# Optimization experiments

Measured on AMD Instinct MI355X. Metric: run time of the kernel, lower is better.

Reference implementation:

```python
import jax, jax.numpy as jnp
import numpy as np

EMB_SZ, NHID, NLAYERS, NTOK = 400, 1150, 3, 32000


def _lstm_layer(x, w_ih, w_hh, b_ih, b_hh):
    # x: [S, B, in]; w_ih: [4H, in]; w_hh: [4H, H]; gate order i, f, g, o (PyTorch)
    S, B, _ = x.shape
    H = w_hh.shape[1]
    # precompute input contributions for all timesteps (one big GEMM)
    xg = jnp.einsum('sbi,gi->sbg', x, w_ih) + b_ih + b_hh  # [S, B, 4H]

    def step(carry, xt):
        h, c = carry
        g = xt + h @ w_hh.T  # [B, 4H]
        i, f, gg, o = jnp.split(g, 4, axis=-1)
        i = jax.nn.sigmoid(i)
        f = jax.nn.sigmoid(f)
        gg = jnp.tanh(gg)
        o = jax.nn.sigmoid(o)
        c = f * c + i * gg
        h = o * jnp.tanh(c)
        return (h, c), h

    init = (jnp.zeros((B, H), x.dtype), jnp.zeros((B, H), x.dtype))
    _, ys = jax.lax.scan(step, init, xg)
    return ys  # [S, B, H]


def setup_inputs() -> dict:
    key = jax.random.key(0)
    ks = jax.random.split(key, 16)
    S, B = 512, 64
    x = jax.random.randint(ks[0], (S, B), 0, NTOK, dtype=jnp.int64) if jax.config.jax_enable_x64 else jax.random.randint(ks[0], (S, B), 0, NTOK, dtype=jnp.int32)
    initrange = 0.1
    emb = jax.random.uniform(ks[1], (NTOK, EMB_SZ), jnp.float32, -initrange, initrange)
    emb = emb.at[1].set(0.0)  # padding_idx = 1
    dims = [(EMB_SZ, NHID), (NHID, NHID), (NHID, EMB_SZ)]  # (input, hidden) per layer
    d = {"x": x, "emb": emb}
    for l, (din, h) in enumerate(dims):
        s = 1.0 / np.sqrt(h)
        d[f"w_ih{l}"] = jax.random.uniform(ks[2 + 4 * l], (4 * h, din), jnp.float32, -s, s)
        d[f"w_hh{l}"] = jax.random.uniform(ks[3 + 4 * l], (4 * h, h), jnp.float32, -s, s)
        d[f"b_ih{l}"] = jax.random.uniform(ks[4 + 4 * l], (4 * h,), jnp.float32, -s, s)
        d[f"b_hh{l}"] = jax.random.uniform(ks[5 + 4 * l], (4 * h,), jnp.float32, -s, s)
    return d


def reference(x, emb, w_ih0, w_hh0, b_ih0, b_hh0, w_ih1, w_hh1, b_ih1, b_hh1, w_ih2, w_hh2, b_ih2, b_hh2):
    # eval mode: embedding dropout / locked dropout / weight-drop are all identity
    h = emb[x]  # [S, B, emb_sz]
    h = _lstm_layer(h, w_ih0, w_hh0, b_ih0, b_hh0)  # [S, B, nhid]
    h = _lstm_layer(h, w_ih1, w_hh1, b_ih1, b_hh1)  # [S, B, nhid]
    h = _lstm_layer(h, w_ih2, w_hh2, b_ih2, b_hh2)  # [S, B, emb_sz]
    return h
```

## Files before the change

### kernel.cpp

```cpp
#include <hip/hip_runtime.h>
#include <stdint.h>

typedef _Float16 f16x8 __attribute__((ext_vector_type(8)));
typedef _Float16 f16x4 __attribute__((ext_vector_type(4)));
typedef float f32x4 __attribute__((ext_vector_type(4)));

static __device__ __forceinline__ float bf2f(unsigned short u) {
  return __uint_as_float(((unsigned int)u) << 16);
}
static __device__ __forceinline__ unsigned short f2bf(float f) {
  unsigned int u = __float_as_uint(f);
  u = (u + 0x7FFFu + ((u >> 16) & 1u)) >> 16;
  return (unsigned short)u;
}
static __device__ __forceinline__ unsigned short f2h(float f) {
  _Float16 h = (_Float16)f;
  return __builtin_bit_cast(unsigned short, h);
}
static __device__ __forceinline__ float h2f(unsigned short b) {
  _Float16 h = __builtin_bit_cast(_Float16, b);
  return (float)h;
}
static __device__ __forceinline__ float sigm(float x) { return 1.0f / (1.0f + __expf(-x)); }
static __device__ __forceinline__ float tanh_fast(float x) {
  float ax = fabsf(x);
  float e = __expf(-2.0f * ax);
  float r = (1.0f - e) / (1.0f + e);
  return copysignf(r, x);
}

__global__ void probe_kernel(const unsigned int* __restrict__ raw, unsigned int* __restrict__ dflag) {
  __shared__ int s;
  int tid = threadIdx.x;
  if (tid == 0) s = 0;
  __syncthreads();
  int v = 0;
  for (int k = 0; k < 4; ++k) {
    unsigned int d = raw[2048 + tid * 4 + k];
    unsigned int lo = d & 0xFFFFu, ex = (lo >> 7) & 0xFFu;
    if (lo == 0u || (ex >= 0x40u && ex <= 0x7Cu)) v++;
  }
  atomicAdd(&s, v);
  __syncthreads();
  if (tid == 0) dflag[0] = (s >= 614) ? 1u : 0u;
}

__global__ void embed_kernel(const int* __restrict__ x, const void* __restrict__ emb,
                             unsigned short* __restrict__ act, const unsigned int* __restrict__ dflag) {
  int idx = blockIdx.x * 256 + threadIdx.x;
  int row = idx / 56, c = idx % 56;
  unsigned short* dst = act + (size_t)row * 448 + c * 8;
  union { uint4 v; unsigned short s[8]; } o;
  if (c < 50) {
    int tok = x[row];
    if (dflag[0]) {
      const unsigned short* e = (const unsigned short*)emb + (size_t)tok * 400 + c * 8;
      union { uint4 v; unsigned short s[8]; } r; r.v = *(const uint4*)e;
#pragma unroll
      for (int k = 0; k < 8; ++k) o.s[k] = f2h(bf2f(r.s[k]));
    } else {
      const float* e = (const float*)emb + (size_t)tok * 400 + c * 8;
      float4 r0 = *(const float4*)e, r1 = *(const float4*)(e + 4);
      const float* p0 = (const float*)&r0; const float* p1 = (const float*)&r1;
#pragma unroll
      for (int k = 0; k < 4; ++k) { o.s[k] = f2h(p0[k]); o.s[4 + k] = f2h(p1[k]); }
    }
  } else {
    o.v.x = o.v.y = o.v.z = o.v.w = 0u;
  }
  *(uint4*)dst = o.v;
}

__global__ void prep_kernel(const void* __restrict__ wih, const void* __restrict__ whh,
                            const void* __restrict__ bih, const void* __restrict__ bhh,
                            unsigned short* __restrict__ WihG, unsigned short* __restrict__ WhhG,
                            float* __restrict__ biasG, int H, int HPo, int din, int dpIn,
                            const unsigned int* __restrict__ dflag) {
  int nb = 4 * HPo, bid = blockIdx.x, tid = threadIdx.x;
  bool isf32 = (dflag[0] == 0u);
  if (bid < 2 * nb) {
    bool ih = bid < nb;
    int j = ih ? bid : bid - nb;
    int i = (j >> 6) * 16 + (j & 15), q = (j >> 4) & 3;
    int cdst = ih ? dpIn : HPo, csrc = ih ? din : H;
    unsigned short* dst = (ih ? WihG : WhhG) + (size_t)j * cdst;
    bool valid = i < H;
    const void* w = ih ? wih : whh;
    for (int m = tid; m < cdst; m += 256) {
      unsigned short v = 0;
      if (valid && m < csrc) {
        if (isf32) v = f2h(((const float*)w)[(size_t)(q * H + i) * csrc + m]);
        else       v = f2h(bf2f(((const unsigned short*)w)[(size_t)(q * H + i) * csrc + m]));
      }
      dst[m] = v;
    }
  } else {
    for (int m = tid; m < nb; m += 256) {
      int i = (m >> 6) * 16 + (m & 15), q = (m >> 4) & 3;
      float v = 0.0f;
      if (i < H) {
        if (isf32) v = ((const float*)bih)[q * H + i] + ((const float*)bhh)[q * H + i];
        else       v = bf2f(((const unsigned short*)bih)[q * H + i]) + bf2f(((const unsigned short*)bhh)[q * H + i]);
      }
      biasG[m] = v;
    }
  }
}

__global__ void unpad_kernel(const unsigned short* __restrict__ act, void* __restrict__ out,
                             const unsigned int* __restrict__ dflag) {
  int idx = blockIdx.x * 256 + threadIdx.x;
  int row = idx / 50, c = idx % 50;
  const unsigned short* src = act + (size_t)row * 448 + c * 8;
  union { uint4 v; unsigned short s[8]; } u; u.v = *(const uint4*)src;
  if (dflag[0]) {
    union { uint4 v; unsigned short s[8]; } o;
#pragma unroll
    for (int k = 0; k < 8; ++k) o.s[k] = f2bf(h2f(u.s[k]));
    *(uint4*)((unsigned short*)out + (size_t)row * 400 + c * 8) = o.v;
  } else {
    float4 o0, o1;
    float* p0 = (float*)&o0; float* p1 = (float*)&o1;
#pragma unroll
    for (int k = 0; k < 4; ++k) { p0[k] = h2f(u.s[k]); p1[k] = h2f(u.s[4 + k]); }
    float* dst = (float*)out + (size_t)row * 400 + c * 8;
    *(float4*)dst = o0; *(float4*)(dst + 4) = o1;
  }
}

__global__ __launch_bounds__(256, 1) void gemm_xw_kernel(
    const unsigned short* __restrict__ A, const unsigned short* __restrict__ B,
    unsigned short* __restrict__ gx, int K, int chrows) {
  __shared__ unsigned short Asm[128 * 32], Bsm[128 * 32];
  const int tid = threadIdx.x, lane = tid & 63, wv = tid >> 6;
  const int bm0 = blockIdx.x * 128, bn0 = blockIdx.y * 128;
  f32x4 acc[2][8] = {};
  const int nkt = K >> 5;
  for (int kt = 0; kt < nkt; ++kt) {
    __syncthreads();
#pragma unroll
    for (int j = 0; j < 2; ++j) {
      int idx = tid * 2 + j, r = idx >> 2, c4 = idx & 3;
      uint4 va = *(const uint4*)(A + (size_t)(bm0 + r) * K + kt * 32 + c4 * 8);
      uint4 vb = *(const uint4*)(B + (size_t)(bn0 + r) * K + kt * 32 + c4 * 8);
      int off = (r * 64 + c4 * 16) ^ ((r & 7) << 4);
      *(uint4*)((char*)Asm + off) = va;
      *(uint4*)((char*)Bsm + off) = vb;
    }
    __syncthreads();
    f16x8 af[2], bf[8];
#pragma unroll
    for (int rt = 0; rt < 2; ++rt) {
      int arow = wv * 32 + rt * 16 + (lane & 15);
      int off = (arow * 64 + ((lane >> 4) << 4)) ^ ((arow & 7) << 4);
      af[rt] = *(const f16x8*)((char*)Asm + off);
    }
#pragma unroll
    for (int ct = 0; ct < 8; ++ct) {
      int brow = ct * 16 + (lane & 15);
      int off = (brow * 64 + ((lane >> 4) << 4)) ^ ((brow & 7) << 4);
      bf[ct] = *(const f16x8*)((char*)Bsm + off);
    }
#pragma unroll
    for (int rt = 0; rt < 2; ++rt)
#pragma unroll
      for (int ct = 0; ct < 8; ++ct)
        acc[rt][ct] = __builtin_amdgcn_mfma_f32_16x16x32_f16(af[rt], bf[ct], acc[rt][ct], 0, 0, 0);
  }
#pragma unroll
  for (int ct = 0; ct < 8; ++ct) {
    int n = bn0 + ct * 16 + (lane & 15);
    int G = n >> 6, c = n & 63;
    int cellcol = (c & 15) * 4 + (c >> 4);
#pragma unroll
    for (int rt = 0; rt < 2; ++rt) {
#pragma unroll
      for (int reg = 0; reg < 4; ++reg) {
        int m = bm0 + wv * 32 + rt * 16 + ((lane >> 4) << 2) + reg;
        gx[((size_t)G * chrows + m) * 64 + cellcol] = f2h(acc[rt][ct][reg]);
      }
    }
  }
}

template <int HP, int KQW, int NQ, int NCNT>
static __device__ __forceinline__ void rec_body(
    const unsigned short* __restrict__ gxAll, unsigned short* __restrict__ actOut,
    const unsigned short* __restrict__ WhhG, const float* __restrict__ biasG,
    unsigned int* __restrict__ cnt, float* __restrict__ cstate,
    int t0, int TS, int chrows) {
  constexpr int NB = HP / 16;
  constexpr unsigned PERQ = (unsigned)(NB / NCNT);
  constexpr int KS = HP / KQW;
  constexpr int KT = KS / 32;
  constexpr int CF = 4 / NQ;
  constexpr int GSTR = 68;
  extern __shared__ char smem[];
  float* Gp = (float*)smem;
  const int tid = threadIdx.x, lane = tid & 63, wv = tid >> 6;
  const int kq = wv % KQW, t2 = wv / KQW;
  const int nq = t2 % NQ, mh = t2 / NQ;
  const int lrow = lane & 15, kc8 = (lane >> 4) << 3;
  const int G = blockIdx.x >> 1, bh = blockIdx.x & 1;
  const int urow = tid >> 4, ui = tid & 15;
  unsigned int* mycnt = cnt + (size_t)bh * 8 * 32;

  float bs[4];
  float creg = 0.0f;
  f16x8 wreg[CF][KT];
  {
    const unsigned short* wbase = WhhG + (size_t)G * 64 * HP + kq * KS + kc8;
#pragma unroll
    for (int cf = 0; cf < CF; ++cf) {
      const unsigned short* wp = wbase + (size_t)((nq * CF + cf) * 16 + lrow) * HP;
#pragma unroll
      for (int kt = 0; kt < KT; ++kt) wreg[cf][kt] = *(const f16x8*)(wp + kt * 32);
    }
#pragma unroll
    for (int q = 0; q < 4; ++q) bs[q] = biasG[G * 64 + q * 16 + ui];
    if (t0 > 0) creg = cstate[(bh * 32 + urow) * HP + G * 16 + ui];
  }
  __syncthreads();

  const int tend = t0 + TS;
  for (int t = t0; t < tend; ++t) {
    if (t > 0) {
      while (true) {
        int ok = 1;
        if (tid < NCNT)
          ok = (__hip_atomic_load(mycnt + tid * 32, __ATOMIC_RELAXED, __HIP_MEMORY_SCOPE_AGENT) >= PERQ * (unsigned)t);
        if (__syncthreads_and(ok)) break;
        __builtin_amdgcn_s_sleep(1);
      }
      asm volatile("" ::: "memory");
    }
    f16x4 gxv = *(const f16x4*)(gxAll + ((size_t)G * chrows + (t - t0) * 64 + bh * 32 + urow) * 64 + ui * 4);
    if (t > 0) {
      f16x8 hv[KT];
      const unsigned short* hp =
          actOut + ((size_t)(t - 1) * 64 + bh * 32 + mh * 16 + lrow) * HP + kq * KS + kc8;
#pragma unroll
      for (int kt = 0; kt < KT; ++kt) hv[kt] = *(const f16x8*)(hp + kt * 32);
      f32x4 a[CF];
#pragma unroll
      for (int cf = 0; cf < CF; ++cf) a[cf] = f32x4{0.f, 0.f, 0.f, 0.f};
#pragma unroll
      for (int kt = 0; kt < KT; ++kt)
#pragma unroll
        for (int cf = 0; cf < CF; ++cf)
          a[cf] = __builtin_amdgcn_mfma_f32_16x16x32_f16(hv[kt], wreg[cf][kt], a[cf], 0, 0, 0);
      const int br = kq * 32 + mh * 16 + (lane >> 4) * 4;
#pragma unroll
      for (int cf = 0; cf < CF; ++cf)
#pragma unroll
        for (int r = 0; r < 4; ++r)
          Gp[(br + r) * GSTR + (nq * CF + cf) * 16 + (lane & 15)] = a[cf][r];
    }
    asm volatile("s_waitcnt lgkmcnt(0)" ::: "memory");
    __builtin_amdgcn_s_barrier();
    __builtin_amdgcn_sched_barrier(0);
    float gi = (float)gxv[0] + bs[0], gf = (float)gxv[1] + bs[1];
    float gg = (float)gxv[2] + bs[2], go = (float)gxv[3] + bs[3];
    if (t > 0) {
#pragma unroll
      for (int k = 0; k < KQW; ++k) {
        const int base = (k * 32 + urow) * GSTR + ui;
        gi += Gp[base];
        gf += Gp[base + 16];
        gg += Gp[base + 32];
        go += Gp[base + 48];
      }
    }
    float ig = sigm(gi), fg = sigm(gf), gt = tanh_fast(gg), og = sigm(go);
    creg = fg * creg + ig * gt;
    unsigned short hb = f2h(og * tanh_fast(creg));
    int other = __shfl_xor((int)hb, 1);
    if ((ui & 1) == 0) {
      unsigned int pk = ((unsigned)hb & 0xFFFFu) | ((unsigned)other << 16);
      __hip_atomic_store((unsigned int*)(actOut + ((size_t)t * 64 + bh * 32 + urow) * HP + G * 16 + ui),
                         pk, __ATOMIC_RELAXED, __HIP_MEMORY_SCOPE_AGENT);
    }
    asm volatile("s_waitcnt vmcnt(0)" ::: "memory");
    __syncthreads();
    if (tid == 0)
      __hip_atomic_fetch_add(mycnt + (G % NCNT) * 32, 1u, __ATOMIC_RELEASE, __HIP_MEMORY_SCOPE_AGENT);
  }
  cstate[(bh * 32 + urow) * HP + G * 16 + ui] = creg;
}

__global__ __launch_bounds__(512, 1) void lstm_rec1152(
    const unsigned short* __restrict__ gxAll, unsigned short* __restrict__ actOut,
    const unsigned short* __restrict__ WhhG, const float* __restrict__ biasG,
    unsigned int* __restrict__ cnt, float* __restrict__ cstate, int t0, int TS, int chrows) {
  rec_body<1152, 4, 1, 8>(gxAll, actOut, WhhG, biasG, cnt, cstate, t0, TS, chrows);
}
__global__ __launch_bounds__(512, 1) void lstm_rec448(
    const unsigned short* __restrict__ gxAll, unsigned short* __restrict__ actOut,
    const unsigned short* __restrict__ WhhG, const float* __restrict__ biasG,
    unsigned int* __restrict__ cnt, float* __restrict__ cstate, int t0, int TS, int chrows) {
  rec_body<448, 2, 2, 4>(gxAll, actOut, WhhG, biasG, cnt, cstate, t0, TS, chrows);
}

extern "C" void kernel_launch(void* const* d_in, const int* in_sizes, int n_in,
                              void* d_out, int out_size, void* d_ws, size_t ws_size,
                              hipStream_t stream) {
  (void)in_sizes; (void)n_in; (void)out_size;
  const int* x = (const int*)d_in[0];
  const void* emb = d_in[1];
  const void* wih[3] = {d_in[2], d_in[6], d_in[10]};
  const void* whh[3] = {d_in[3], d_in[7], d_in[11]};
  const void* bih[3] = {d_in[4], d_in[8], d_in[12]};
  const void* bhh[3] = {d_in[5], d_in[9], d_in[13]};

  char* ws = (char*)d_ws;
  size_t off = 0;
  unsigned short* act0 = (unsigned short*)(ws + off); off += (size_t)32768 * 448 * 2;
  unsigned short* act1 = (unsigned short*)(ws + off); off += (size_t)32768 * 1152 * 2;
  unsigned short* act2 = (unsigned short*)(ws + off); off += (size_t)32768 * 1152 * 2;
  unsigned short* act3 = act0;
  unsigned short* WihG = (unsigned short*)(ws + off); off += (size_t)4608 * 1152 * 2;
  unsigned short* WhhG = (unsigned short*)(ws + off); off += (size_t)4608 * 1152 * 2;
  float* biasG = (float*)(ws + off); off += (size_t)4608 * 4;
  float* cstate = (float*)(ws + off); off += (size_t)64 * 1152 * 4;
  unsigned int* cnt = (unsigned int*)(ws + off); off += 4096;
  unsigned int* dflag = (unsigned int*)(ws + off); off += 256;
  unsigned short* gx = (unsigned short*)(ws + off);

  size_t avail = (ws_size > off) ? (ws_size - off) : 0;
  int CH = 512;
  while (CH > 32 && (size_t)CH * 589824 > avail) CH >>= 1;
  const int chrows = CH * 64, nch = 512 / CH;

  const size_t lds1152 = 128 * 68 * 4;
  const size_t lds448 = 64 * 68 * 4;

  probe_kernel<<<1, 256, 0, stream>>>((const unsigned int*)emb, dflag);
  embed_kernel<<<7168, 256, 0, stream>>>(x, emb, act0, dflag);

  prep_kernel<<<2 * 4608 + 1, 256, 0, stream>>>(wih[0], whh[0], bih[0], bhh[0],
                                                WihG, WhhG, biasG, 1150, 1152, 400, 448, dflag);
  hipMemsetAsync(cnt, 0, 4096, stream);
  for (int c = 0; c < nch; ++c) {
    gemm_xw_kernel<<<dim3(CH / 2, 36), 256, 0, stream>>>(act0 + (size_t)c * chrows * 448, WihG, gx, 448, chrows);
    lstm_rec1152<<<144, 512, lds1152, stream>>>(gx, act1, WhhG, biasG, cnt, cstate, c * CH, CH, chrows);
  }

  prep_kernel<<<2 * 4608 + 1, 256, 0, stream>>>(wih[1], whh[1], bih[1], bhh[1],
                                                WihG, WhhG, biasG, 1150, 1152, 1150, 1152, dflag);
  hipMemsetAsync(cnt, 0, 4096, stream);
  for (int c = 0; c < nch; ++c) {
    gemm_xw_kernel<<<dim3(CH / 2, 36), 256, 0, stream>>>(act1 + (size_t)c * chrows * 1152, WihG, gx, 1152, chrows);
    lstm_rec1152<<<144, 512, lds1152, stream>>>(gx, act2, WhhG, biasG, cnt, cstate, c * CH, CH, chrows);
  }

  prep_kernel<<<2 * 1792 + 1, 256, 0, stream>>>(wih[2], whh[2], bih[2], bhh[2],
                                                WihG, WhhG, biasG, 400, 448, 1150, 1152, dflag);
  hipMemsetAsync(cnt, 0, 4096, stream);
  for (int c = 0; c < nch; ++c) {
    gemm_xw_kernel<<<dim3(CH / 2, 14), 256, 0, stream>>>(act2 + (size_t)c * chrows * 1152, WihG, gx, 1152, chrows);
    lstm_rec448<<<56, 512, lds448, stream>>>(gx, act3, WhhG, biasG, cnt, cstate, c * CH, CH, chrows);
  }

  unpad_kernel<<<6400, 256, 0, stream>>>(act3, d_out, dflag);
}
```

Measured before the change: 10.04 ms.

## Split batch into four 16-row quarters and pipeline recurrent LSTM halves per block

Each recurrent block now handles two 16-row batch quarters instead of one 32-row half. All 8 waves split K across all 4 gates, and quarters A and B are processed in a staggered way. Quarter B's hidden-state loads and MFMA overlap with quarter A's gate reduction and counter signaling, so dependent blocks can start sooner. This adds extra barriers, counter polls and LDS traffic per timestep, and uses an uneven K split (4/5 or 2/1 k-tiles per wave) that can leave waves imbalanced.

New measurement: 11.34 ms. 1.13x slower.

```diff
diff --git a/kernel.cpp b/kernel.cpp
--- a/kernel.cpp
+++ b/kernel.cpp
@@ -183,88 +183,94 @@
   }
 }
 
-template <int HP, int KQW, int NQ, int NCNT>
+template <int KT>
+static __device__ __forceinline__ void loadh(f16x8* hv, const unsigned short* hp) {
+#pragma unroll
+  for (int kt = 0; kt < KT; ++kt) hv[kt] = *(const f16x8*)(hp + kt * 32);
+}
+template <int KT, int KTM>
+static __device__ __forceinline__ void loadw(f16x8 wreg[4][KTM], const unsigned short* wp, int HP) {
+#pragma unroll
+  for (int cf = 0; cf < 4; ++cf)
+#pragma unroll
+    for (int kt = 0; kt < KT; ++kt)
+      wreg[cf][kt] = *(const f16x8*)(wp + (size_t)cf * 16 * HP + kt * 32);
+}
+template <int KT, int KTM>
+static __device__ __forceinline__ void mmaq(const f16x8* hv, const f16x8 wreg[4][KTM], f32x4 acc[4]) {
+#pragma unroll
+  for (int kt = 0; kt < KT; ++kt)
+#pragma unroll
+    for (int cf = 0; cf < 4; ++cf)
+      acc[cf] = __builtin_amdgcn_mfma_f32_16x16x32_f16(hv[kt], wreg[cf][kt], acc[cf], 0, 0, 0);
+}
+
+template <int HP, int NA, int KTa, int KTb, int NCNT>
 static __device__ __forceinline__ void rec_body(
     const unsigned short* __restrict__ gxAll, unsigned short* __restrict__ actOut,
     const unsigned short* __restrict__ WhhG, const float* __restrict__ biasG,
     unsigned int* __restrict__ cnt, float* __restrict__ cstate,
-    int t0, int TS, int chrows) {
-  constexpr int NB = HP / 16;
-  constexpr unsigned PERQ = (unsigned)(NB / NCNT);
-  constexpr int KS = HP / KQW;
-  constexpr int KT = KS / 32;
-  constexpr int CF = 4 / NQ;
-  constexpr int GSTR = 68;
+    int t0, int TS, int chrows, int bid) {
+  constexpr int NGRP = HP / 16;
+  constexpr unsigned PERQ = (unsigned)(NGRP / NCNT);
+  constexpr int KTM = (KTa > KTb) ? KTa : KTb;
+  constexpr int GSTR = 72;
   extern __shared__ char smem[];
   float* Gp = (float*)smem;
   const int tid = threadIdx.x, lane = tid & 63, wv = tid >> 6;
-  const int kq = wv % KQW, t2 = wv / KQW;
-  const int nq = t2 % NQ, mh = t2 / NQ;
   const int lrow = lane & 15, kc8 = (lane >> 4) << 3;
-  const int G = blockIdx.x >> 1, bh = blockIdx.x & 1;
-  const int urow = tid >> 4, ui = tid & 15;
-  unsigned int* mycnt = cnt + (size_t)bh * 8 * 32;
-
-  float bs[4];
-  float creg = 0.0f;
-  f16x8 wreg[CF][KT];
+  const int G = bid >> 1, pr = bid & 1;
+  const int qa = pr * 2, qb = pr * 2 + 1;
+  const int kq = wv;
+  const int k0 = (kq < NA) ? kq * KTa * 32 : NA * KTa * 32 + (kq - NA) * KTb * 32;
+  const bool red = tid < 256;
+  const int urow = (tid >> 4) & 15, ui = tid & 15;
+  unsigned int* cntA = cnt + qa * 256;
+  unsigned int* cntB = cnt + qb * 256;
+
+  f16x8 wreg[4][KTM];
   {
-    const unsigned short* wbase = WhhG + (size_t)G * 64 * HP + kq * KS + kc8;
-#pragma unroll
-    for (int cf = 0; cf < CF; ++cf) {
-      const unsigned short* wp = wbase + (size_t)((nq * CF + cf) * 16 + lrow) * HP;
-#pragma unroll
-      for (int kt = 0; kt < KT; ++kt) wreg[cf][kt] = *(const f16x8*)(wp + kt * 32);
-    }
+    const unsigned short* wp = WhhG + ((size_t)(G * 64 + lrow)) * HP + k0 + kc8;
+    if (kq < NA) loadw<KTa, KTM>(wreg, wp, HP);
+    else         loadw<KTb, KTM>(wreg, wp, HP);
+  }
+  float bs[4] = {0.f, 0.f, 0.f, 0.f};
+  float cA = 0.f, cB = 0.f;
+  if (red) {
 #pragma unroll
     for (int q = 0; q < 4; ++q) bs[q] = biasG[G * 64 + q * 16 + ui];
-    if (t0 > 0) creg = cstate[(bh * 32 + urow) * HP + G * 16 + ui];
+    if (t0 > 0) {
+      cA = cstate[(qa * 16 + urow) * HP + G * 16 + ui];
+      cB = cstate[(qb * 16 + urow) * HP + G * 16 + ui];
+    }
   }
   __syncthreads();
 
-  const int tend = t0 + TS;
-  for (int t = t0; t < tend; ++t) {
-    if (t > 0) {
-      while (true) {
-        int ok = 1;
-        if (tid < NCNT)
-          ok = (__hip_atomic_load(mycnt + tid * 32, __ATOMIC_RELAXED, __HIP_MEMORY_SCOPE_AGENT) >= PERQ * (unsigned)t);
-        if (__syncthreads_and(ok)) break;
-        __builtin_amdgcn_s_sleep(1);
-      }
-      asm volatile("" ::: "memory");
-    }
-    f16x4 gxv = *(const f16x4*)(gxAll + ((size_t)G * chrows + (t - t0) * 64 + bh * 32 + urow) * 64 + ui * 4);
-    if (t > 0) {
-      f16x8 hv[KT];
-      const unsigned short* hp =
-          actOut + ((size_t)(t - 1) * 64 + bh * 32 + mh * 16 + lrow) * HP + kq * KS + kc8;
-#pragma unroll
-      for (int kt = 0; kt < KT; ++kt) hv[kt] = *(const f16x8*)(hp + kt * 32);
-      f32x4 a[CF];
-#pragma unroll
-      for (int cf = 0; cf < CF; ++cf) a[cf] = f32x4{0.f, 0.f, 0.f, 0.f};
-#pragma unroll
-      for (int kt = 0; kt < KT; ++kt)
-#pragma unroll
-        for (int cf = 0; cf < CF; ++cf)
-          a[cf] = __builtin_amdgcn_mfma_f32_16x16x32_f16(hv[kt], wreg[cf][kt], a[cf], 0, 0, 0);
-      const int br = kq * 32 + mh * 16 + (lane >> 4) * 4;
-#pragma unroll
-      for (int cf = 0; cf < CF; ++cf)
-#pragma unroll
-        for (int r = 0; r < 4; ++r)
-          Gp[(br + r) * GSTR + (nq * CF + cf) * 16 + (lane & 15)] = a[cf][r];
-    }
-    asm volatile("s_waitcnt lgkmcnt(0)" ::: "memory");
-    __builtin_amdgcn_s_barrier();
-    __builtin_amdgcn_sched_barrier(0);
+  auto pollq = [&](unsigned int* cq, unsigned need) {
+    while (true) {
+      int ok = 1;
+      if (tid < NCNT)
+        ok = (__hip_atomic_load(cq + tid * 32, __ATOMIC_RELAXED, __HIP_MEMORY_SCOPE_AGENT) >= need);
+      if (__syncthreads_and(ok)) break;
+      __builtin_amdgcn_s_sleep(1);
+    }
+    asm volatile("" ::: "memory");
+  };
+  auto stGp = [&](f32x4 acc[4]) {
+    const int br = kq * 16 + (lane >> 4) * 4;
+#pragma unroll
+    for (int cf = 0; cf < 4; ++cf)
+#pragma unroll
+      for (int r = 0; r < 4; ++r)
+        Gp[(br + r) * GSTR + cf * 16 + lrow] = acc[cf][r];
+  };
+  auto reduceq = [&](int q, int t, float& cc, f16x4 gxv, bool useGp) {
     float gi = (float)gxv[0] + bs[0], gf = (float)gxv[1] + bs[1];
     float gg = (float)gxv[2] + bs[2], go = (float)gxv[3] + bs[3];
-    if (t > 0) {
-#pragma unroll
-      for (int k = 0; k < KQW; ++k) {
-        const int base = (k * 32 + urow) * GSTR + ui;
+    if (useGp) {
+#pragma unroll
+      for (int k = 0; k < 8; ++k) {
+        const int base = (k * 16 + urow) * GSTR + ui;
         gi += Gp[base];
         gf += Gp[base + 16];
         gg += Gp[base + 32];
@@ -272,33 +278,78 @@
       }
     }
     float ig = sigm(gi), fg = sigm(gf), gt = tanh_fast(gg), og = sigm(go);
-    creg = fg * creg + ig * gt;
-    unsigned short hb = f2h(og * tanh_fast(creg));
+    cc = fg * cc + ig * gt;
+    unsigned short hb = f2h(og * tanh_fast(cc));
     int other = __shfl_xor((int)hb, 1);
     if ((ui & 1) == 0) {
       unsigned int pk = ((unsigned)hb & 0xFFFFu) | ((unsigned)other << 16);
-      __hip_atomic_store((unsigned int*)(actOut + ((size_t)t * 64 + bh * 32 + urow) * HP + G * 16 + ui),
+      __hip_atomic_store((unsigned int*)(actOut + ((size_t)t * 64 + q * 16 + urow) * HP + G * 16 + ui),
                          pk, __ATOMIC_RELAXED, __HIP_MEMORY_SCOPE_AGENT);
     }
+  };
+
+  const int tend = t0 + TS;
+  for (int t = t0; t < tend; ++t) {
+    const int tr = t - t0;
+    if (t > 0) pollq(cntA, PERQ * (unsigned)t);
+    f16x4 gxa = {}, gxb = {};
+    if (red) {
+      gxa = *(const f16x4*)(gxAll + ((size_t)G * chrows + tr * 64 + qa * 16 + urow) * 64 + ui * 4);
+      gxb = *(const f16x4*)(gxAll + ((size_t)G * chrows + tr * 64 + qb * 16 + urow) * 64 + ui * 4);
+    }
+    if (t > 0) {
+      f16x8 hv[KTM];
+      const unsigned short* hpA = actOut + ((size_t)(t - 1) * 64 + qa * 16 + lrow) * HP + k0 + kc8;
+      f32x4 acc[4] = {};
+      if (kq < NA) { loadh<KTa>(hv, hpA); mmaq<KTa, KTM>(hv, wreg, acc); }
+      else         { loadh<KTb>(hv, hpA); mmaq<KTb, KTM>(hv, wreg, acc); }
+      stGp(acc);
+    }
+    if (t > 0) pollq(cntB, PERQ * (unsigned)t);
+    else __syncthreads();
+    f16x8 hvB[KTM];
+    if (t > 0) {
+      const unsigned short* hpB = actOut + ((size_t)(t - 1) * 64 + qb * 16 + lrow) * HP + k0 + kc8;
+      if (kq < NA) loadh<KTa>(hvB, hpB);
+      else         loadh<KTb>(hvB, hpB);
+    }
+    if (red) reduceq(qa, t, cA, gxa, t > 0);
     asm volatile("s_waitcnt vmcnt(0)" ::: "memory");
     __syncthreads();
     if (tid == 0)
-      __hip_atomic_fetch_add(mycnt + (G % NCNT) * 32, 1u, __ATOMIC_RELEASE, __HIP_MEMORY_SCOPE_AGENT);
-  }
-  cstate[(bh * 32 + urow) * HP + G * 16 + ui] = creg;
+      __hip_atomic_fetch_add(cntA + (G & (NCNT - 1)) * 32, 1u, __ATOMIC_RELEASE, __HIP_MEMORY_SCOPE_AGENT);
+    if (t > 0) {
+      f32x4 acc[4] = {};
+      if (kq < NA) mmaq<KTa, KTM>(hvB, wreg, acc);
+      else         mmaq<KTb, KTM>(hvB, wreg, acc);
+      stGp(acc);
+    }
+    asm volatile("s_waitcnt lgkmcnt(0)" ::: "memory");
+    __builtin_amdgcn_s_barrier();
+    __builtin_amdgcn_sched_barrier(0);
+    if (red) reduceq(qb, t, cB, gxb, t > 0);
+    asm volatile("s_waitcnt vmcnt(0)" ::: "memory");
+    __syncthreads();
+    if (tid == 0)
+      __hip_atomic_fetch_add(cntB + (G & (NCNT - 1)) * 32, 1u, __ATOMIC_RELEASE, __HIP_MEMORY_SCOPE_AGENT);
+  }
+  if (red) {
+    cstate[(qa * 16 + urow) * HP + G * 16 + ui] = cA;
+    cstate[(qb * 16 + urow) * HP + G * 16 + ui] = cB;
+  }
 }
 
 __global__ __launch_bounds__(512, 1) void lstm_rec1152(
     const unsigned short* __restrict__ gxAll, unsigned short* __restrict__ actOut,
     const unsigned short* __restrict__ WhhG, const float* __restrict__ biasG,
     unsigned int* __restrict__ cnt, float* __restrict__ cstate, int t0, int TS, int chrows) {
-  rec_body<1152, 4, 1, 8>(gxAll, actOut, WhhG, biasG, cnt, cstate, t0, TS, chrows);
+  rec_body<1152, 4, 4, 5, 8>(gxAll, actOut, WhhG, biasG, cnt, cstate, t0, TS, chrows, blockIdx.x);
 }
 __global__ __launch_bounds__(512, 1) void lstm_rec448(
     const unsigned short* __restrict__ gxAll, unsigned short* __restrict__ actOut,
     const unsigned short* __restrict__ WhhG, const float* __restrict__ biasG,
     unsigned int* __restrict__ cnt, float* __restrict__ cstate, int t0, int TS, int chrows) {
-  rec_body<448, 2, 2, 4>(gxAll, actOut, WhhG, biasG, cnt, cstate, t0, TS, chrows);
+  rec_body<448, 6, 2, 1, 4>(gxAll, actOut, WhhG, biasG, cnt, cstate, t0, TS, chrows, blockIdx.x);
 }
 
 extern "C" void kernel_launch(void* const* d_in, const int* in_sizes, int n_in,
@@ -331,8 +382,7 @@
   while (CH > 32 && (size_t)CH * 589824 > avail) CH >>= 1;
   const int chrows = CH * 64, nch = 512 / CH;
 
-  const size_t lds1152 = 128 * 68 * 4;
-  const size_t lds448 = 64 * 68 * 4;
+  const size_t ldsrec = 128 * 72 * 4;
 
   probe_kernel<<<1, 256, 0, stream>>>((const unsigned int*)emb, dflag);
   embed_kernel<<<7168, 256, 0, stream>>>(x, emb, act0, dflag);
@@ -342,7 +392,7 @@
   hipMemsetAsync(cnt, 0, 4096, stream);
   for (int c = 0; c < nch; ++c) {
     gemm_xw_kernel<<<dim3(CH / 2, 36), 256, 0, stream>>>(act0 + (size_t)c * chrows * 448, WihG, gx, 448, chrows);
-    lstm_rec1152<<<144, 512, lds1152, stream>>>(gx, act1, WhhG, biasG, cnt, cstate, c * CH, CH, chrows);
+    lstm_rec1152<<<144, 512, ldsrec, stream>>>(gx, act1, WhhG, biasG, cnt, cstate, c * CH, CH, chrows);
   }
 
   prep_kernel<<<2 * 4608 + 1, 256, 0, stream>>>(wih[1], whh[1], bih[1], bhh[1],
@@ -350,7 +400,7 @@
   hipMemsetAsync(cnt, 0, 4096, stream);
   for (int c = 0; c < nch; ++c) {
     gemm_xw_kernel<<<dim3(CH / 2, 36), 256, 0, stream>>>(act1 + (size_t)c * chrows * 1152, WihG, gx, 1152, chrows);
-    lstm_rec1152<<<144, 512, lds1152, stream>>>(gx, act2, WhhG, biasG, cnt, cstate, c * CH, CH, chrows);
+    lstm_rec1152<<<144, 512, ldsrec, stream>>>(gx, act2, WhhG, biasG, cnt, cstate, c * CH, CH, chrows);
   }
 
   prep_kernel<<<2 * 1792 + 1, 256, 0, stream>>>(wih[2], whh[2], bih[2], bhh[2],
@@ -358,7 +408,7 @@
   hipMemsetAsync(cnt, 0, 4096, stream);
   for (int c = 0; c < nch; ++c) {
     gemm_xw_kernel<<<dim3(CH / 2, 14), 256, 0, stream>>>(act2 + (size_t)c * chrows * 1152, WihG, gx, 1152, chrows);
-    lstm_rec448<<<56, 512, lds448, stream>>>(gx, act3, WhhG, biasG, cnt, cstate, c * CH, CH, chrows);
+    lstm_rec448<<<56, 512, ldsrec, stream>>>(gx, act3, WhhG, biasG, cnt, cstate, c * CH, CH, chrows);
   }
 
   unpad_kernel<<<6400, 256, 0, stream>>>(act3, d_out, dflag);
```

## Repartition 1152-wide LSTM recurrence into 24-unit groups across 192 blocks

Applied to the files above, without the earlier changes.

The 1152-hidden recurrent kernel is rewritten so each block owns 24 hidden units (96 gate rows) for a 16-row batch quarter, giving 192 blocks instead of 144. All 8 waves split the K dimension unevenly (160/128) and hold the weights in registers, and the partial sums are reduced through a larger static LDS tile. The weight, bias and gx layouts are generalized to a configurable group width, so prep and the input GEMM emit a 96-wide gate interleave for layers 0 and 1. The aim is more CUs working on each sequential timestep and more work per wave. In exchange it uses more register pressure and more sync counters per step, and the batch quarters now each need their own barrier.

Result: no change. 9.896 ms (-1.4%).

```diff
diff --git a/kernel.cpp b/kernel.cpp
--- a/kernel.cpp
+++ b/kernel.cpp
@@ -74,14 +74,16 @@
 __global__ void prep_kernel(const void* __restrict__ wih, const void* __restrict__ whh,
                             const void* __restrict__ bih, const void* __restrict__ bhh,
                             unsigned short* __restrict__ WihG, unsigned short* __restrict__ WhhG,
-                            float* __restrict__ biasG, int H, int HPo, int din, int dpIn,
+                            float* __restrict__ biasG, int H, int HPo, int din, int dpIn, int GW,
                             const unsigned int* __restrict__ dflag) {
   int nb = 4 * HPo, bid = blockIdx.x, tid = threadIdx.x;
+  int upg = GW >> 2;
   bool isf32 = (dflag[0] == 0u);
   if (bid < 2 * nb) {
     bool ih = bid < nb;
     int j = ih ? bid : bid - nb;
-    int i = (j >> 6) * 16 + (j & 15), q = (j >> 4) & 3;
+    int rj = j % GW;
+    int i = (j / GW) * upg + rj % upg, q = rj / upg;
     int cdst = ih ? dpIn : HPo, csrc = ih ? din : H;
     unsigned short* dst = (ih ? WihG : WhhG) + (size_t)j * cdst;
     bool valid = i < H;
@@ -96,7 +98,8 @@
     }
   } else {
     for (int m = tid; m < nb; m += 256) {
-      int i = (m >> 6) * 16 + (m & 15), q = (m >> 4) & 3;
+      int rj = m % GW;
+      int i = (m / GW) * upg + rj % upg, q = rj / upg;
       float v = 0.0f;
       if (i < H) {
         if (isf32) v = ((const float*)bih)[q * H + i] + ((const float*)bhh)[q * H + i];
@@ -130,10 +133,11 @@
 
 __global__ __launch_bounds__(256, 1) void gemm_xw_kernel(
     const unsigned short* __restrict__ A, const unsigned short* __restrict__ B,
-    unsigned short* __restrict__ gx, int K, int chrows) {
+    unsigned short* __restrict__ gx, int K, int chrows, int GW) {
   __shared__ unsigned short Asm[128 * 32], Bsm[128 * 32];
   const int tid = threadIdx.x, lane = tid & 63, wv = tid >> 6;
   const int bm0 = blockIdx.x * 128, bn0 = blockIdx.y * 128;
+  const int upg = GW >> 2;
   f32x4 acc[2][8] = {};
   const int nkt = K >> 5;
   for (int kt = 0; kt < nkt; ++kt) {
@@ -170,55 +174,57 @@
 #pragma unroll
   for (int ct = 0; ct < 8; ++ct) {
     int n = bn0 + ct * 16 + (lane & 15);
-    int G = n >> 6, c = n & 63;
-    int cellcol = (c & 15) * 4 + (c >> 4);
+    int G = n / GW, c = n % GW;
+    int cellcol = (c % upg) * 4 + (c / upg);
 #pragma unroll
     for (int rt = 0; rt < 2; ++rt) {
 #pragma unroll
       for (int reg = 0; reg < 4; ++reg) {
         int m = bm0 + wv * 32 + rt * 16 + ((lane >> 4) << 2) + reg;
-        gx[((size_t)G * chrows + m) * 64 + cellcol] = f2h(acc[rt][ct][reg]);
-      }
-    }
-  }
-}
-
-template <int HP, int KQW, int NQ, int NCNT>
-static __device__ __forceinline__ void rec_body(
+        gx[((size_t)G * chrows + m) * GW + cellcol] = f2h(acc[rt][ct][reg]);
+      }
+    }
+  }
+}
+
+__global__ __launch_bounds__(512, 1) void lstm_rec1152(
     const unsigned short* __restrict__ gxAll, unsigned short* __restrict__ actOut,
     const unsigned short* __restrict__ WhhG, const float* __restrict__ biasG,
     unsigned int* __restrict__ cnt, float* __restrict__ cstate,
     int t0, int TS, int chrows) {
-  constexpr int NB = HP / 16;
-  constexpr unsigned PERQ = (unsigned)(NB / NCNT);
-  constexpr int KS = HP / KQW;
-  constexpr int KT = KS / 32;
-  constexpr int CF = 4 / NQ;
-  constexpr int GSTR = 68;
-  extern __shared__ char smem[];
-  float* Gp = (float*)smem;
+  constexpr int HP = 1152, GSTR = 100;
+  __shared__ float Gp[128 * GSTR];
   const int tid = threadIdx.x, lane = tid & 63, wv = tid >> 6;
-  const int kq = wv % KQW, t2 = wv / KQW;
-  const int nq = t2 % NQ, mh = t2 / NQ;
   const int lrow = lane & 15, kc8 = (lane >> 4) << 3;
-  const int G = blockIdx.x >> 1, bh = blockIdx.x & 1;
-  const int urow = tid >> 4, ui = tid & 15;
-  unsigned int* mycnt = cnt + (size_t)bh * 8 * 32;
-
-  float bs[4];
+  const int G = blockIdx.x >> 2, rq = blockIdx.x & 3;
+  const int k0 = (wv < 4) ? wv * 160 : 640 + (wv - 4) * 128;
+  const int urow = tid >> 5, ui = tid & 31;
+  const bool red = ui < 24;
+  unsigned int* mycnt = cnt + rq * 256;
+
+  f16x8 wreg[6][5];
+  {
+    const unsigned short* wp = WhhG + ((size_t)(G * 96 + lrow)) * HP + k0 + kc8;
+    if (wv < 4) {
+#pragma unroll
+      for (int cf = 0; cf < 6; ++cf)
+#pragma unroll
+        for (int kt = 0; kt < 5; ++kt)
+          wreg[cf][kt] = *(const f16x8*)(wp + (size_t)cf * 16 * HP + kt * 32);
+    } else {
+#pragma unroll
+      for (int cf = 0; cf < 6; ++cf)
+#pragma unroll
+        for (int kt = 0; kt < 4; ++kt)
+          wreg[cf][kt] = *(const f16x8*)(wp + (size_t)cf * 16 * HP + kt * 32);
+    }
+  }
+  float bs[4] = {0.f, 0.f, 0.f, 0.f};
   float creg = 0.0f;
-  f16x8 wreg[CF][KT];
-  {
-    const unsigned short* wbase = WhhG + (size_t)G * 64 * HP + kq * KS + kc8;
-#pragma unroll
-    for (int cf = 0; cf < CF; ++cf) {
-      const unsigned short* wp = wbase + (size_t)((nq * CF + cf) * 16 + lrow) * HP;
-#pragma unroll
-      for (int kt = 0; kt < KT; ++kt) wreg[cf][kt] = *(const f16x8*)(wp + kt * 32);
-    }
-#pragma unroll
-    for (int q = 0; q < 4; ++q) bs[q] = biasG[G * 64 + q * 16 + ui];
-    if (t0 > 0) creg = cstate[(bh * 32 + urow) * HP + G * 16 + ui];
+  if (red) {
+#pragma unroll
+    for (int q = 0; q < 4; ++q) bs[q] = biasG[G * 96 + q * 24 + ui];
+    if (t0 > 0) creg = cstate[(rq * 16 + urow) * HP + G * 24 + ui];
   }
   __syncthreads();
 
@@ -227,8 +233,117 @@
     if (t > 0) {
       while (true) {
         int ok = 1;
-        if (tid < NCNT)
-          ok = (__hip_atomic_load(mycnt + tid * 32, __ATOMIC_RELAXED, __HIP_MEMORY_SCOPE_AGENT) >= PERQ * (unsigned)t);
+        if (tid < 8)
+          ok = (__hip_atomic_load(mycnt + tid * 32, __ATOMIC_RELAXED, __HIP_MEMORY_SCOPE_AGENT) >= 6u * (unsigned)t);
+        if (__syncthreads_and(ok)) break;
+        __builtin_amdgcn_s_sleep(1);
+      }
+      asm volatile("" ::: "memory");
+    }
+    f16x4 gxv = {};
+    if (red)
+      gxv = *(const f16x4*)(gxAll + ((size_t)G * chrows + (t - t0) * 64 + rq * 16 + urow) * 96 + ui * 4);
+    if (t > 0) {
+      f16x8 hv[5];
+      const unsigned short* hp = actOut + ((size_t)(t - 1) * 64 + rq * 16 + lrow) * HP + k0 + kc8;
+      f32x4 acc[6] = {};
+      if (wv < 4) {
+#pragma unroll
+        for (int kt = 0; kt < 5; ++kt) hv[kt] = *(const f16x8*)(hp + kt * 32);
+#pragma unroll
+        for (int kt = 0; kt < 5; ++kt)
+#pragma unroll
+          for (int cf = 0; cf < 6; ++cf)
+            acc[cf] = __builtin_amdgcn_mfma_f32_16x16x32_f16(hv[kt], wreg[cf][kt], acc[cf], 0, 0, 0);
+      } else {
+#pragma unroll
+        for (int kt = 0; kt < 4; ++kt) hv[kt] = *(const f16x8*)(hp + kt * 32);
+#pragma unroll
+        for (int kt = 0; kt < 4; ++kt)
+#pragma unroll
+          for (int cf = 0; cf < 6; ++cf)
+            acc[cf] = __builtin_amdgcn_mfma_f32_16x16x32_f16(hv[kt], wreg[cf][kt], acc[cf], 0, 0, 0);
+      }
+      const int br = (lane >> 4) * 4;
+#pragma unroll
+      for (int cf = 0; cf < 6; ++cf)
+#pragma unroll
+        for (int r = 0; r < 4; ++r)
+          Gp[(wv * 16 + br + r) * GSTR + cf * 16 + lrow] = acc[cf][r];
+    }
+    asm volatile("s_waitcnt lgkmcnt(0)" ::: "memory");
+    __builtin_amdgcn_s_barrier();
+    __builtin_amdgcn_sched_barrier(0);
+    if (red) {
+      float gi = (float)gxv[0] + bs[0], gf = (float)gxv[1] + bs[1];
+      float gg = (float)gxv[2] + bs[2], go = (float)gxv[3] + bs[3];
+      if (t > 0) {
+#pragma unroll
+        for (int k = 0; k < 8; ++k) {
+          const int base = (k * 16 + urow) * GSTR + ui;
+          gi += Gp[base];
+          gf += Gp[base + 24];
+          gg += Gp[base + 48];
+          go += Gp[base + 72];
+        }
+      }
+      float ig = sigm(gi), fg = sigm(gf), gt = tanh_fast(gg), og = sigm(go);
+      creg = fg * creg + ig * gt;
+      unsigned short hb = f2h(og * tanh_fast(creg));
+      int other = __shfl_xor((int)hb, 1);
+      if ((ui & 1) == 0) {
+        unsigned int pk = ((unsigned)hb & 0xFFFFu) | ((unsigned)other << 16);
+        __hip_atomic_store((unsigned int*)(actOut + ((size_t)t * 64 + rq * 16 + urow) * HP + G * 24 + ui),
+                           pk, __ATOMIC_RELAXED, __HIP_MEMORY_SCOPE_AGENT);
+      }
+    }
+    asm volatile("s_waitcnt vmcnt(0)" ::: "memory");
+    __syncthreads();
+    if (tid == 0)
+      __hip_atomic_fetch_add(mycnt + (G & 7) * 32, 1u, __ATOMIC_RELEASE, __HIP_MEMORY_SCOPE_AGENT);
+  }
+  if (red) cstate[(rq * 16 + urow) * HP + G * 24 + ui] = creg;
+}
+
+__global__ __launch_bounds__(512, 1) void lstm_rec448(
+    const unsigned short* __restrict__ gxAll, unsigned short* __restrict__ actOut,
+    const unsigned short* __restrict__ WhhG, const float* __restrict__ biasG,
+    unsigned int* __restrict__ cnt, float* __restrict__ cstate,
+    int t0, int TS, int chrows) {
+  constexpr int HP = 448, GSTR = 68, KT = 7;
+  __shared__ float Gp[64 * GSTR];
+  const int tid = threadIdx.x, lane = tid & 63, wv = tid >> 6;
+  const int kq = wv & 1, t2 = wv >> 1;
+  const int nq = t2 & 1, mh = t2 >> 1;
+  const int lrow = lane & 15, kc8 = (lane >> 4) << 3;
+  const int G = blockIdx.x >> 1, bh = blockIdx.x & 1;
+  const int urow = tid >> 4, ui = tid & 15;
+  unsigned int* mycnt = cnt + (size_t)bh * 256;
+
+  float bs[4];
+  float creg = 0.0f;
+  f16x8 wreg[2][KT];
+  {
+    const unsigned short* wbase = WhhG + (size_t)G * 64 * HP + kq * 224 + kc8;
+#pragma unroll
+    for (int cf = 0; cf < 2; ++cf) {
+      const unsigned short* wp = wbase + (size_t)((nq * 2 + cf) * 16 + lrow) * HP;
+#pragma unroll
+      for (int kt = 0; kt < KT; ++kt) wreg[cf][kt] = *(const f16x8*)(wp + kt * 32);
+    }
+#pragma unroll
+    for (int q = 0; q < 4; ++q) bs[q] = biasG[G * 64 + q * 16 + ui];
+    if (t0 > 0) creg = cstate[(bh * 32 + urow) * HP + G * 16 + ui];
+  }
+  __syncthreads();
+
+  const int tend = t0 + TS;
+  for (int t = t0; t < tend; ++t) {
+    if (t > 0) {
+      while (true) {
+        int ok = 1;
+        if (tid < 4)
+          ok = (__hip_atomic_load(mycnt + tid * 32, __ATOMIC_RELAXED, __HIP_MEMORY_SCOPE_AGENT) >= 7u * (unsigned)t);
         if (__syncthreads_and(ok)) break;
         __builtin_amdgcn_s_sleep(1);
       }
@@ -238,23 +353,21 @@
     if (t > 0) {
       f16x8 hv[KT];
       const unsigned short* hp =
-          actOut + ((size_t)(t - 1) * 64 + bh * 32 + mh * 16 + lrow) * HP + kq * KS + kc8;
+          actOut + ((size_t)(t - 1) * 64 + bh * 32 + mh * 16 + lrow) * HP + kq * 224 + kc8;
 #pragma unroll
       for (int kt = 0; kt < KT; ++kt) hv[kt] = *(const f16x8*)(hp + kt * 32);
-      f32x4 a[CF];
-#pragma unroll
-      for (int cf = 0; cf < CF; ++cf) a[cf] = f32x4{0.f, 0.f, 0.f, 0.f};
+      f32x4 a[2] = {};
 #pragma unroll
       for (int kt = 0; kt < KT; ++kt)
 #pragma unroll
-        for (int cf = 0; cf < CF; ++cf)
+        for (int cf = 0; cf < 2; ++cf)
           a[cf] = __builtin_amdgcn_mfma_f32_16x16x32_f16(hv[kt], wreg[cf][kt], a[cf], 0, 0, 0);
       const int br = kq * 32 + mh * 16 + (lane >> 4) * 4;
 #pragma unroll
-      for (int cf = 0; cf < CF; ++cf)
+      for (int cf = 0; cf < 2; ++cf)
 #pragma unroll
         for (int r = 0; r < 4; ++r)
-          Gp[(br + r) * GSTR + (nq * CF + cf) * 16 + (lane & 15)] = a[cf][r];
+          Gp[(br + r) * GSTR + (nq * 2 + cf) * 16 + lrow] = a[cf][r];
     }
     asm volatile("s_waitcnt lgkmcnt(0)" ::: "memory");
     __builtin_amdgcn_s_barrier();
@@ -263,7 +376,7 @@
     float gg = (float)gxv[2] + bs[2], go = (float)gxv[3] + bs[3];
     if (t > 0) {
 #pragma unroll
-      for (int k = 0; k < KQW; ++k) {
+      for (int k = 0; k < 2; ++k) {
         const int base = (k * 32 + urow) * GSTR + ui;
         gi += Gp[base];
         gf += Gp[base + 16];
@@ -283,22 +396,9 @@
     asm volatile("s_waitcnt vmcnt(0)" ::: "memory");
     __syncthreads();
     if (tid == 0)
-      __hip_atomic_fetch_add(mycnt + (G % NCNT) * 32, 1u, __ATOMIC_RELEASE, __HIP_MEMORY_SCOPE_AGENT);
+      __hip_atomic_fetch_add(mycnt + (G & 3) * 32, 1u, __ATOMIC_RELEASE, __HIP_MEMORY_SCOPE_AGENT);
   }
   cstate[(bh * 32 + urow) * HP + G * 16 + ui] = creg;
-}
-
-__global__ __launch_bounds__(512, 1) void lstm_rec1152(
-    const unsigned short* __restrict__ gxAll, unsigned short* __restrict__ actOut,
-    const unsigned short* __restrict__ WhhG, const float* __restrict__ biasG,
-    unsigned int* __restrict__ cnt, float* __restrict__ cstate, int t0, int TS, int chrows) {
-  rec_body<1152, 4, 1, 8>(gxAll, actOut, WhhG, biasG, cnt, cstate, t0, TS, chrows);
-}
-__global__ __launch_bounds__(512, 1) void lstm_rec448(
-    const unsigned short* __restrict__ gxAll, unsigned short* __restrict__ actOut,
-    const unsigned short* __restrict__ WhhG, const float* __restrict__ biasG,
-    unsigned int* __restrict__ cnt, float* __restrict__ cstate, int t0, int TS, int chrows) {
-  rec_body<448, 2, 2, 4>(gxAll, actOut, WhhG, biasG, cnt, cstate, t0, TS, chrows);
 }
 
 extern "C" void kernel_launch(void* const* d_in, const int* in_sizes, int n_in,
@@ -331,34 +431,31 @@
   while (CH > 32 && (size_t)CH * 589824 > avail) CH >>= 1;
   const int chrows = CH * 64, nch = 512 / CH;
 
-  const size_t lds1152 = 128 * 68 * 4;
-  const size_t lds448 = 64 * 68 * 4;
-
   probe_kernel<<<1, 256, 0, stream>>>((const unsigned int*)emb, dflag);
   embed_kernel<<<7168, 256, 0, stream>>>(x, emb, act0, dflag);
 
   prep_kernel<<<2 * 4608 + 1, 256, 0, stream>>>(wih[0], whh[0], bih[0], bhh[0],
-                                                WihG, WhhG, biasG, 1150, 1152, 400, 448, dflag);
+                                                WihG, WhhG, biasG, 1150, 1152, 400, 448, 96, dflag);
   hipMemsetAsync(cnt, 0, 4096, stream);
   for (int c = 0; c < nch; ++c) {
-    gemm_xw_kernel<<<dim3(CH / 2, 36), 256, 0, stream>>>(act0 + (size_t)c * chrows * 448, WihG, gx, 448, chrows);
-    lstm_rec1152<<<144, 512, lds1152, stream>>>(gx, act1, WhhG, biasG, cnt, cstate, c * CH, CH, chrows);
+    gemm_xw_kernel<<<dim3(CH / 2, 36), 256, 0, stream>>>(act0 + (size_t)c * chrows * 448, WihG, gx, 448, chrows, 96);
+    lstm_rec1152<<<192, 512, 0, stream>>>(gx, act1, WhhG, biasG, cnt, cstate, c * CH, CH, chrows);
   }
 
   prep_kernel<<<2 * 4608 + 1, 256, 0, stream>>>(wih[1], whh[1], bih[1], bhh[1],
-                                                WihG, WhhG, biasG, 1150, 1152, 1150, 1152, dflag);
+                                                WihG, WhhG, biasG, 1150, 1152, 1150, 1152, 96, dflag);
   hipMemsetAsync(cnt, 0, 4096, stream);
   for (int c = 0; c < nch; ++c) {
-    gemm_xw_kernel<<<dim3(CH / 2, 36), 256, 0, stream>>>(act1 + (size_t)c * chrows * 1152, WihG, gx, 1152, chrows);
-    lstm_rec1152<<<144, 512, lds1152, stream>>>(gx, act2, WhhG, biasG, cnt, cstate, c * CH, CH, chrows);
+    gemm_xw_kernel<<<dim3(CH / 2, 36), 256, 0, stream>>>(act1 + (size_t)c * chrows * 1152, WihG, gx, 1152, chrows, 96);
+    lstm_rec1152<<<192, 512, 0, stream>>>(gx, act2, WhhG, biasG, cnt, cstate, c * CH, CH, chrows);
   }
 
   prep_kernel<<<2 * 1792 + 1, 256, 0, stream>>>(wih[2], whh[2], bih[2], bhh[2],
-                                                WihG, WhhG, biasG, 400, 448, 1150, 1152, dflag);
+                                                WihG, WhhG, biasG, 400, 448, 1150, 1152, 64, dflag);
   hipMemsetAsync(cnt, 0, 4096, stream);
   for (int c = 0; c < nch; ++c) {
-    gemm_xw_kernel<<<dim3(CH / 2, 14), 256, 0, stream>>>(act2 + (size_t)c * chrows * 1152, WihG, gx, 1152, chrows);
-    lstm_rec448<<<56, 512, lds448, stream>>>(gx, act3, WhhG, biasG, cnt, cstate, c * CH, CH, chrows);
+    gemm_xw_kernel<<<dim3(CH / 2, 14), 256, 0, stream>>>(act2 + (size_t)c * chrows * 1152, WihG, gx, 1152, chrows, 64);
+    lstm_rec448<<<56, 512, 0, stream>>>(gx, act3, WhhG, biasG, cnt, cstate, c * CH, CH, chrows);
   }
 
   unpad_kernel<<<6400, 256, 0, stream>>>(act3, d_out, dflag);
```
